# Kernel optimization log

Measured on AMD Instinct MI355X. Metric: run time of the kernel, lower is better.

Reference implementation:

```python
import jax, jax.numpy as jnp
import numpy as np
import math

EMBED = 512
HEADS = 2
HEAD_DIM = EMBED // HEADS
EPS = 1e-5

def layer_norm(x, g, b):
    mu = jnp.mean(x, axis=-1, keepdims=True)
    var = jnp.var(x, axis=-1, keepdims=True)
    return (x - mu) * jax.lax.rsqrt(var + EPS) * g + b

def setup_inputs() -> dict:
    key = jax.random.key(0)
    ks = jax.random.split(key, 16)
    s = 0.02
    inp = {
        "text_embeds": jax.random.normal(ks[0], (128, 32, EMBED), jnp.float32),
        "video_embeds": jax.random.normal(ks[1], (64, 12, EMBED), jnp.float32),
        "ln1_g": jnp.ones((EMBED,), jnp.float32),
        "ln1_b": jnp.zeros((EMBED,), jnp.float32),
        "Wq": jax.random.normal(ks[2], (EMBED, EMBED), jnp.float32) * s,
        "bq": jnp.zeros((EMBED,), jnp.float32),
        "Wk": jax.random.normal(ks[3], (EMBED, EMBED), jnp.float32) * s,
        "bk": jnp.zeros((EMBED,), jnp.float32),
        "Wv": jax.random.normal(ks[4], (EMBED, EMBED), jnp.float32) * s,
        "bv": jnp.zeros((EMBED,), jnp.float32),
        "Wo": jax.random.normal(ks[5], (EMBED, EMBED), jnp.float32) * s,
        "bo": jnp.zeros((EMBED,), jnp.float32),
        "Wl": jax.random.normal(ks[6], (EMBED, EMBED), jnp.float32) * s,
        "bl": jnp.zeros((EMBED,), jnp.float32),
        "ln2_g": jnp.ones((EMBED,), jnp.float32),
        "ln2_b": jnp.zeros((EMBED,), jnp.float32),
        "ln3_g": jnp.ones((EMBED,), jnp.float32),
        "ln3_b": jnp.zeros((EMBED,), jnp.float32),
    }
    return inp

def reference(text_embeds, video_embeds, ln1_g, ln1_b, Wq, bq, Wk, bk, Wv, bv,
              Wo, bo, Wl, bl, ln2_g, ln2_b, ln3_g, ln3_b):
    # shared layer_norm1 on both modalities
    t = layer_norm(text_embeds, ln1_g, ln1_b)    # [T, Nw, E]
    vd = layer_norm(video_embeds, ln1_g, ln1_b)  # [V, F, E]
    T, Nw, _ = t.shape
    V, Fr, _ = vd.shape
    q = (t @ Wq.T + bq).reshape(T, Nw, HEADS, HEAD_DIM)   # bthd
    k = (vd @ Wk.T + bk).reshape(V, Fr, HEADS, HEAD_DIM)  # avhd
    v = (vd @ Wv.T + bv).reshape(V, Fr, HEADS, HEAD_DIM)  # avhd
    # cross-modal outer-product attention logits: [V, T, H, F, Nw]
    logits = jnp.einsum('avhd,bthd->abhvt', k, q) / math.sqrt(HEAD_DIM)
    weights = jax.nn.softmax(logits, axis=3)  # softmax over frames
    attn = jnp.einsum('avhd,abhvt->abhtd', v, weights)  # [V, T, H, Nw, D]
    attn = attn.transpose(0, 1, 3, 2, 4).reshape(V, T, Nw, EMBED)
    attn = attn.mean(axis=0)                    # [T, Nw, E]
    o = attn @ Wo.T + bo
    o = layer_norm(o, ln2_g, ln2_b)
    lin = o @ Wl.T + bl  # dropout is identity in eval mode
    out = layer_norm(o + lin, ln3_g, ln3_b)
    return out
```

## Files before the change

kernel.cpp:

```cpp
#include <hip/hip_runtime.h>
#include <math.h>

#define EMBED 512
#define HD 256
#define FR 12
#define NV 64
#define NT_TOK 4096
#define NV_TOK 768

typedef __attribute__((ext_vector_type(8))) short short8;
typedef __attribute__((ext_vector_type(4))) float f32x4;

__device__ __forceinline__ unsigned int f2bf(float f) {
  unsigned int u = __float_as_uint(f);
  u += 0x7FFFu + ((u >> 16) & 1u);
  return u >> 16;
}
__device__ __forceinline__ void async_cp16(void* lds, const void* g) {
  __builtin_amdgcn_global_load_lds(
      (const __attribute__((address_space(1))) void*)g,
      (__attribute__((address_space(3))) void*)lds, 16, 0, 0);
}

__device__ __forceinline__ void gemm64_core(
    const unsigned short* __restrict__ Ab, int lda,
    const unsigned short* __restrict__ Bb, int ldb,
    int m0, int n0, int K,
    unsigned short* __restrict__ As, unsigned short* __restrict__ Bs,
    f32x4 acc[2][2]) {
  int tid = threadIdx.x;
  int w = tid >> 6, lane = tid & 63;
  int lr = lane & 15, quad = lane >> 4;
  int wm = (w >> 1) * 32, wn = (w & 1) * 32;
  int rowS[2], cgS[2];
  #pragma unroll
  for (int i = 0; i < 2; ++i) {
    int s = tid + i * 256;
    rowS[i] = s >> 3; cgS[i] = (s & 7) ^ (rowS[i] & 7);
  }
  int nk = K >> 6;
  #pragma unroll
  for (int i = 0; i < 2; ++i) {
    async_cp16(&As[(tid + i * 256) * 8],
               Ab + (size_t)(m0 + rowS[i]) * lda + cgS[i] * 8);
    async_cp16(&Bs[(tid + i * 256) * 8],
               Bb + (size_t)(n0 + rowS[i]) * ldb + cgS[i] * 8);
  }
  for (int k = 0; k < nk; ++k) {
    int cur = k & 1;
    __syncthreads();
    if (k + 1 < nk) {
      int nxt = cur ^ 1, koff = (k + 1) << 6;
      #pragma unroll
      for (int i = 0; i < 2; ++i) {
        async_cp16(&As[nxt * 4096 + (tid + i * 256) * 8],
                   Ab + (size_t)(m0 + rowS[i]) * lda + koff + cgS[i] * 8);
        async_cp16(&Bs[nxt * 4096 + (tid + i * 256) * 8],
                   Bb + (size_t)(n0 + rowS[i]) * ldb + koff + cgS[i] * 8);
      }
    }
    const unsigned short* Ac = As + cur * 4096;
    const unsigned short* Bc = Bs + cur * 4096;
    #pragma unroll
    for (int kk = 0; kk < 2; ++kk) {
      int sw = ((kk * 4 + quad) ^ (lr & 7)) * 8;
      short8 a0 = *(const short8*)&Ac[(wm + lr) * 64 + sw];
      short8 a1 = *(const short8*)&Ac[(wm + 16 + lr) * 64 + sw];
      short8 b0 = *(const short8*)&Bc[(wn + lr) * 64 + sw];
      short8 b1 = *(const short8*)&Bc[(wn + 16 + lr) * 64 + sw];
      acc[0][0] = __builtin_amdgcn_mfma_f32_16x16x32_bf16(a0, b0, acc[0][0], 0, 0, 0);
      acc[0][1] = __builtin_amdgcn_mfma_f32_16x16x32_bf16(a0, b1, acc[0][1], 0, 0, 0);
      acc[1][0] = __builtin_amdgcn_mfma_f32_16x16x32_bf16(a1, b0, acc[1][0], 0, 0, 0);
      acc[1][1] = __builtin_amdgcn_mfma_f32_16x16x32_bf16(a1, b1, acc[1][1], 0, 0, 0);
    }
  }
}

template <int MODE, bool BIAS>
__global__ __launch_bounds__(256, 4) void gemm64(
    const unsigned short* __restrict__ A, int lda, long AzS,
    const unsigned short* __restrict__ B, int ldb, long BzS,
    const float* __restrict__ bias, void* __restrict__ Cv, int ldc, long CzS,
    int K) {
  __shared__ __align__(16) unsigned short As[2 * 4096];
  __shared__ __align__(16) unsigned short Bs[2 * 4096];
  f32x4 acc[2][2] = {};
  const unsigned short* Ab = A + (size_t)blockIdx.z * AzS;
  const unsigned short* Bb = B + (size_t)blockIdx.z * BzS;
  int m0 = blockIdx.x * 64, n0 = blockIdx.y * 64;
  gemm64_core(Ab, lda, Bb, ldb, m0, n0, K, As, Bs, acc);
  int w = threadIdx.x >> 6, lane = threadIdx.x & 63;
  int lr = lane & 15, quad = lane >> 4;
  int wm = (w >> 1) * 32, wn = (w & 1) * 32;
  long cz = (long)blockIdx.z * CzS;
  #pragma unroll
  for (int j = 0; j < 2; ++j) {
    int col = n0 + wn + j * 16 + lr;
    float bv = BIAS ? bias[col] : 0.0f;
    #pragma unroll
    for (int i = 0; i < 2; ++i) {
      int rbase = m0 + wm + i * 16 + quad * 4;
      #pragma unroll
      for (int r = 0; r < 4; ++r) {
        float v = acc[i][j][r] + bv;
        if (MODE == 0)
          ((unsigned short*)Cv)[cz + (size_t)(rbase + r) * ldc + col] =
              (unsigned short)f2bf(v);
        else
          ((float*)Cv)[cz + (size_t)(rbase + r) * ldc + col] = v;
      }
    }
  }
}

__global__ __launch_bounds__(256, 4) void qkv_kernel(
    const unsigned short* __restrict__ tn, const unsigned short* __restrict__ vn,
    const unsigned short* __restrict__ Wq, const unsigned short* __restrict__ Wk,
    const unsigned short* __restrict__ Wv,
    const float* __restrict__ bq, const float* __restrict__ bk,
    const float* __restrict__ bv,
    unsigned short* __restrict__ Q, unsigned short* __restrict__ Kout,
    unsigned short* __restrict__ V) {
  __shared__ __align__(16) unsigned short As[2 * 4096];
  __shared__ __align__(16) unsigned short Bs[2 * 4096];
  int bid = blockIdx.x;
  const unsigned short *Ap, *Bp;
  const float* bias;
  unsigned short* outp;
  int m0, n0;
  if (bid < 512) {
    Ap = tn; Bp = Wq; bias = bq; outp = Q;
    m0 = (bid >> 3) * 64; n0 = (bid & 7) * 64;
  } else if (bid < 608) {
    int i = bid - 512;
    Ap = vn; Bp = Wk; bias = bk; outp = Kout;
    m0 = (i >> 3) * 64; n0 = (i & 7) * 64;
  } else {
    int i = bid - 608;
    Ap = vn; Bp = Wv; bias = bv; outp = V;
    m0 = (i >> 3) * 64; n0 = (i & 7) * 64;
  }
  f32x4 acc[2][2] = {};
  gemm64_core(Ap, EMBED, Bp, EMBED, m0, n0, EMBED, As, Bs, acc);
  int w = threadIdx.x >> 6, lane = threadIdx.x & 63;
  int lr = lane & 15, quad = lane >> 4;
  int wm = (w >> 1) * 32, wn = (w & 1) * 32;
  #pragma unroll
  for (int j = 0; j < 2; ++j) {
    int col = n0 + wn + j * 16 + lr;
    float bvv = bias[col];
    #pragma unroll
    for (int i = 0; i < 2; ++i) {
      int rbase = m0 + wm + i * 16 + quad * 4;
      #pragma unroll
      for (int r = 0; r < 4; ++r)
        outp[(size_t)(rbase + r) * EMBED + col] =
            (unsigned short)f2bf(acc[i][j][r] + bvv);
    }
  }
}

__global__ __launch_bounds__(256, 4) void sgemm_softmax(
    const unsigned short* __restrict__ Q, const unsigned short* __restrict__ Kb,
    const unsigned short* __restrict__ V, const unsigned short* __restrict__ Wo,
    unsigned short* __restrict__ P, unsigned short* __restrict__ W2) {
  __shared__ __align__(16) char smem[40960];
  int tid = threadIdx.x;
  int w = tid >> 6, lane = tid & 63;
  int lr = lane & 15, quad = lane >> 4;
  int bid = blockIdx.x;

  if (bid >= 1024) {
    int j = bid - 1024;
    int h = j / 96, i = j % 96;
    int m0 = (i / 12) * 64, n0 = (i % 12) * 64;
    unsigned short* As = (unsigned short*)smem;
    unsigned short* Bs = (unsigned short*)(smem + 16384);
    f32x4 acc[2][2] = {};
    gemm64_core(Wo + h * HD, EMBED, V + h * HD, EMBED, m0, n0, HD, As, Bs, acc);
    int wm = (w >> 1) * 32, wn = (w & 1) * 32;
    #pragma unroll
    for (int j2 = 0; j2 < 2; ++j2) {
      int col = n0 + wn + j2 * 16 + lr;
      #pragma unroll
      for (int i2 = 0; i2 < 2; ++i2) {
        int rbase = m0 + wm + i2 * 16 + quad * 4;
        #pragma unroll
        for (int r = 0; r < 4; ++r)
          W2[(size_t)(rbase + r) * 1536 + h * 768 + col] =
              (unsigned short)f2bf(acc[i2][j2][r]);
      }
    }
    return;
  }

  unsigned short* As = (unsigned short*)smem;
  unsigned short* Bs = (unsigned short*)(smem + 16384);
  int wm = (w >> 1) * 32, wn = (w & 1) * 48;
  int h = bid >> 9, rem = bid & 511;
  int m0 = (rem >> 3) * 64, n0 = (rem & 7) * 96;
  const unsigned short* Ab = Q + h * HD;
  const unsigned short* Bb = Kb + h * HD;
  int rowA[2], cgA[2], rowB[3], cgB[3];
  #pragma unroll
  for (int i = 0; i < 2; ++i) {
    int s = tid + i * 256;
    rowA[i] = s >> 3; cgA[i] = (s & 7) ^ (rowA[i] & 7);
  }
  #pragma unroll
  for (int i = 0; i < 3; ++i) {
    int s = tid + i * 256;
    rowB[i] = s >> 3; cgB[i] = (s & 7) ^ (rowB[i] & 7);
  }
  f32x4 acc[2][3] = {};
  const int nk = HD >> 6;
  #pragma unroll
  for (int i = 0; i < 2; ++i)
    async_cp16(&As[(tid + i * 256) * 8],
               Ab + (size_t)(m0 + rowA[i]) * EMBED + cgA[i] * 8);
  #pragma unroll
  for (int i = 0; i < 3; ++i)
    async_cp16(&Bs[(tid + i * 256) * 8],
               Bb + (size_t)(n0 + rowB[i]) * EMBED + cgB[i] * 8);
  for (int k = 0; k < nk; ++k) {
    int cur = k & 1;
    __syncthreads();
    if (k + 1 < nk) {
      int nxt = cur ^ 1, koff = (k + 1) << 6;
      #pragma unroll
      for (int i = 0; i < 2; ++i)
        async_cp16(&As[nxt * 4096 + (tid + i * 256) * 8],
                   Ab + (size_t)(m0 + rowA[i]) * EMBED + koff + cgA[i] * 8);
      #pragma unroll
      for (int i = 0; i < 3; ++i)
        async_cp16(&Bs[nxt * 6144 + (tid + i * 256) * 8],
                   Bb + (size_t)(n0 + rowB[i]) * EMBED + koff + cgB[i] * 8);
    }
    const unsigned short* Ac = As + cur * 4096;
    const unsigned short* Bc = Bs + cur * 6144;
    #pragma unroll
    for (int kk = 0; kk < 2; ++kk) {
      int sw = ((kk * 4 + quad) ^ (lr & 7)) * 8;
      short8 a0 = *(const short8*)&Ac[(wm + lr) * 64 + sw];
      short8 a1 = *(const short8*)&Ac[(wm + 16 + lr) * 64 + sw];
      short8 b0 = *(const short8*)&Bc[(wn + lr) * 64 + sw];
      short8 b1 = *(const short8*)&Bc[(wn + 16 + lr) * 64 + sw];
      short8 b2 = *(const short8*)&Bc[(wn + 32 + lr) * 64 + sw];
      acc[0][0] = __builtin_amdgcn_mfma_f32_16x16x32_bf16(a0, b0, acc[0][0], 0, 0, 0);
      acc[0][1] = __builtin_amdgcn_mfma_f32_16x16x32_bf16(a0, b1, acc[0][1], 0, 0, 0);
      acc[0][2] = __builtin_amdgcn_mfma_f32_16x16x32_bf16(a0, b2, acc[0][2], 0, 0, 0);
      acc[1][0] = __builtin_amdgcn_mfma_f32_16x16x32_bf16(a1, b0, acc[1][0], 0, 0, 0);
      acc[1][1] = __builtin_amdgcn_mfma_f32_16x16x32_bf16(a1, b1, acc[1][1], 0, 0, 0);
      acc[1][2] = __builtin_amdgcn_mfma_f32_16x16x32_bf16(a1, b2, acc[1][2], 0, 0, 0);
    }
  }
  __syncthreads();
  float* Sx = (float*)smem;
  #pragma unroll
  for (int j = 0; j < 3; ++j) {
    int col = wn + j * 16 + lr;
    #pragma unroll
    for (int i = 0; i < 2; ++i) {
      int rbase = wm + i * 16 + quad * 4;
      #pragma unroll
      for (int r = 0; r < 4; ++r) Sx[(rbase + r) * 100 + col] = acc[i][j][r];
    }
  }
  __syncthreads();
  #pragma unroll
  for (int gi = 0; gi < 2; ++gi) {
    int g = tid * 2 + gi;
    int row = g >> 3, gr = g & 7;
    const float* sp = Sx + row * 100 + gr * 12;
    float v[12];
    float m = -1e30f;
    #pragma unroll
    for (int f = 0; f < FR; ++f) { v[f] = sp[f] * 0.0625f; m = fmaxf(m, v[f]); }
    float s = 0.f;
    #pragma unroll
    for (int f = 0; f < FR; ++f) { v[f] = __expf(v[f] - m); s += v[f]; }
    float inv = (1.0f / NV) / s;
    unsigned short* pp =
        P + (size_t)(m0 + row) * 1536 + h * 768 + n0 + gr * 12;
    #pragma unroll
    for (int ii = 0; ii < 6; ++ii) {
      unsigned int lo = f2bf(v[2 * ii] * inv), hi = f2bf(v[2 * ii + 1] * inv);
      *(unsigned int*)(pp + 2 * ii) = lo | (hi << 16);
    }
  }
}

__device__ __forceinline__ void ln_row(
    const float* __restrict__ xr, const float* __restrict__ rr,
    const float* __restrict__ g, const float* __restrict__ b,
    float* __restrict__ outf, unsigned short* __restrict__ outb) {
  int t = threadIdx.x;
  float v0 = xr[t], v1 = xr[t + 256];
  if (rr != nullptr) { v0 += rr[t]; v1 += rr[t + 256]; }
  float s = v0 + v1;
  float s2 = v0 * v0 + v1 * v1;
  #pragma unroll
  for (int off = 32; off > 0; off >>= 1) {
    s += __shfl_down(s, off, 64);
    s2 += __shfl_down(s2, off, 64);
  }
  __shared__ float ss[4], ss2[4];
  __shared__ float mean_s, rstd_s;
  int wid = t >> 6;
  if ((t & 63) == 0) { ss[wid] = s; ss2[wid] = s2; }
  __syncthreads();
  if (t == 0) {
    float a = ss[0] + ss[1] + ss[2] + ss[3];
    float a2 = ss2[0] + ss2[1] + ss2[2] + ss2[3];
    float mean = a * (1.0f / EMBED);
    float var = a2 * (1.0f / EMBED) - mean * mean;
    mean_s = mean;
    rstd_s = rsqrtf(var + 1e-5f);
  }
  __syncthreads();
  float mean = mean_s, rstd = rstd_s;
  float y0 = (v0 - mean) * rstd * g[t] + b[t];
  float y1 = (v1 - mean) * rstd * g[t + 256] + b[t + 256];
  if (outf != nullptr) { outf[t] = y0; outf[t + 256] = y1; }
  if (outb != nullptr) {
    outb[t] = (unsigned short)f2bf(y0);
    outb[t + 256] = (unsigned short)f2bf(y1);
  }
}

__global__ __launch_bounds__(256) void ln_kernel(
    const float* __restrict__ x, const float* __restrict__ res,
    const float* __restrict__ g, const float* __restrict__ b,
    float* __restrict__ outf, unsigned short* __restrict__ outb) {
  size_t row = blockIdx.x;
  ln_row(x + row * EMBED, res ? res + row * EMBED : nullptr, g, b,
         outf ? outf + row * EMBED : nullptr,
         outb ? outb + row * EMBED : nullptr);
}

__global__ __launch_bounds__(256) void prep_kernel(
    const float* __restrict__ text, const float* __restrict__ video,
    const float* __restrict__ g, const float* __restrict__ b,
    const float* __restrict__ Wq, const float* __restrict__ Wk,
    const float* __restrict__ Wv, const float* __restrict__ Wo,
    const float* __restrict__ Wl, unsigned short* __restrict__ Wbf,
    unsigned short* __restrict__ tn, unsigned short* __restrict__ vn) {
  int bid = blockIdx.x;
  if (bid < 1280) {
    int i = bid * 256 + threadIdx.x;
    const float* srcs[5] = {Wq, Wk, Wv, Wo, Wl};
    const float* src = srcs[i >> 16];
    float4 v = ((const float4*)src)[i & 65535];
    uint2 o;
    o.x = f2bf(v.x) | (f2bf(v.y) << 16);
    o.y = f2bf(v.z) | (f2bf(v.w) << 16);
    ((uint2*)Wbf)[i] = o;
    return;
  }
  if (bid < 1280 + NT_TOK) {
    size_t row = bid - 1280;
    ln_row(text + row * EMBED, nullptr, g, b, nullptr, tn + row * EMBED);
  } else {
    size_t row = bid - (1280 + NT_TOK);
    ln_row(video + row * EMBED, nullptr, g, b, nullptr, vn + row * EMBED);
  }
}

extern "C" void kernel_launch(void* const* d_in, const int* in_sizes, int n_in,
                              void* d_out, int out_size, void* d_ws, size_t ws_size,
                              hipStream_t stream) {
  (void)in_sizes; (void)n_in; (void)out_size; (void)ws_size;
  const float* text  = (const float*)d_in[0];
  const float* video = (const float*)d_in[1];
  const float* ln1_g = (const float*)d_in[2];
  const float* ln1_b = (const float*)d_in[3];
  const float* Wq = (const float*)d_in[4];
  const float* bq = (const float*)d_in[5];
  const float* Wk = (const float*)d_in[6];
  const float* bk = (const float*)d_in[7];
  const float* Wv = (const float*)d_in[8];
  const float* bv = (const float*)d_in[9];
  const float* Wo = (const float*)d_in[10];
  const float* bo = (const float*)d_in[11];
  const float* Wl = (const float*)d_in[12];
  const float* bl = (const float*)d_in[13];
  const float* ln2_g = (const float*)d_in[14];
  const float* ln2_b = (const float*)d_in[15];
  const float* ln3_g = (const float*)d_in[16];
  const float* ln3_b = (const float*)d_in[17];
  float* out = (float*)d_out;

  char* base = (char*)d_ws;
  unsigned short* Wbf   = (unsigned short*)base;
  unsigned short* Wq_bf = Wbf + 0 * 262144;
  unsigned short* Wk_bf = Wbf + 1 * 262144;
  unsigned short* Wv_bf = Wbf + 2 * 262144;
  unsigned short* Wo_bf = Wbf + 3 * 262144;
  unsigned short* Wl_bf = Wbf + 4 * 262144;
  unsigned short* W2    = (unsigned short*)(base + 2621440);
  unsigned short* tn_bf = (unsigned short*)(base + 4194304);
  unsigned short* vn_bf = (unsigned short*)(base + 8388608);
  unsigned short* Q_bf  = (unsigned short*)(base + 9175040);
  unsigned short* K_bf  = (unsigned short*)(base + 13369344);
  unsigned short* V_bf  = (unsigned short*)(base + 14155776);
  unsigned short* P     = (unsigned short*)(base + 14942208);
  float* Ob  = (float*)(base + 4194304);
  float* o2f = (float*)(base + 14942208);
  unsigned short* o2_bf = (unsigned short*)(base + 23330816);
  float* lin = (float*)(base + 4194304);

  prep_kernel<<<1280 + NT_TOK + NV_TOK, 256, 0, stream>>>(
      text, video, ln1_g, ln1_b, Wq, Wk, Wv, Wo, Wl, Wbf, tn_bf, vn_bf);

  qkv_kernel<<<704, 256, 0, stream>>>(tn_bf, vn_bf, Wq_bf, Wk_bf, Wv_bf,
                                      bq, bk, bv, Q_bf, K_bf, V_bf);

  sgemm_softmax<<<1216, 256, 0, stream>>>(Q_bf, K_bf, V_bf, Wo_bf, P, W2);

  gemm64<1, true><<<dim3(64, 8, 1), 256, 0, stream>>>(
      P, 1536, 0, W2, 1536, 0, bo, Ob, EMBED, 0, 1536);

  ln_kernel<<<NT_TOK, 256, 0, stream>>>(Ob, nullptr, ln2_g, ln2_b, o2f, o2_bf);
  gemm64<1, true><<<dim3(64, 8, 1), 256, 0, stream>>>(
      o2_bf, EMBED, 0, Wl_bf, EMBED, 0, bl, lin, EMBED, 0, EMBED);
  ln_kernel<<<NT_TOK, 256, 0, stream>>>(o2f, lin, ln3_g, ln3_b, out, nullptr);
}
```

Before: 164.2 us.

## Fuse LN2 stats into Wo GEMM epilogue and LN2 apply into Wl GEMM

The Wo projection GEMM now accumulates per-row sum and sum-of-squares into a stats buffer with atomics, and the buffer is zeroed inside the QKV kernel. The Wl GEMM normalizes its fp32 input on the fly while staging the A tile, so the standalone LN2 kernel and its fp32/bf16 intermediates go away. The final LN3 kernel recomputes the LN2 output from Ob and the stats. This removes one launch and a full pass over activations, at the cost of global atomics, redundant LN2 work across the 8 column blocks, synchronous A-tile loads in the Wl GEMM, and a one-pass variance formula.

After: 161.5 us. About the same (-1.7%).

```diff
diff --git a/kernel.cpp b/kernel.cpp
--- a/kernel.cpp
+++ b/kernel.cpp
@@ -76,43 +76,6 @@
   }
 }
 
-template <int MODE, bool BIAS>
-__global__ __launch_bounds__(256, 4) void gemm64(
-    const unsigned short* __restrict__ A, int lda, long AzS,
-    const unsigned short* __restrict__ B, int ldb, long BzS,
-    const float* __restrict__ bias, void* __restrict__ Cv, int ldc, long CzS,
-    int K) {
-  __shared__ __align__(16) unsigned short As[2 * 4096];
-  __shared__ __align__(16) unsigned short Bs[2 * 4096];
-  f32x4 acc[2][2] = {};
-  const unsigned short* Ab = A + (size_t)blockIdx.z * AzS;
-  const unsigned short* Bb = B + (size_t)blockIdx.z * BzS;
-  int m0 = blockIdx.x * 64, n0 = blockIdx.y * 64;
-  gemm64_core(Ab, lda, Bb, ldb, m0, n0, K, As, Bs, acc);
-  int w = threadIdx.x >> 6, lane = threadIdx.x & 63;
-  int lr = lane & 15, quad = lane >> 4;
-  int wm = (w >> 1) * 32, wn = (w & 1) * 32;
-  long cz = (long)blockIdx.z * CzS;
-  #pragma unroll
-  for (int j = 0; j < 2; ++j) {
-    int col = n0 + wn + j * 16 + lr;
-    float bv = BIAS ? bias[col] : 0.0f;
-    #pragma unroll
-    for (int i = 0; i < 2; ++i) {
-      int rbase = m0 + wm + i * 16 + quad * 4;
-      #pragma unroll
-      for (int r = 0; r < 4; ++r) {
-        float v = acc[i][j][r] + bv;
-        if (MODE == 0)
-          ((unsigned short*)Cv)[cz + (size_t)(rbase + r) * ldc + col] =
-              (unsigned short)f2bf(v);
-        else
-          ((float*)Cv)[cz + (size_t)(rbase + r) * ldc + col] = v;
-      }
-    }
-  }
-}
-
 __global__ __launch_bounds__(256, 4) void qkv_kernel(
     const unsigned short* __restrict__ tn, const unsigned short* __restrict__ vn,
     const unsigned short* __restrict__ Wq, const unsigned short* __restrict__ Wk,
@@ -120,10 +83,11 @@
     const float* __restrict__ bq, const float* __restrict__ bk,
     const float* __restrict__ bv,
     unsigned short* __restrict__ Q, unsigned short* __restrict__ Kout,
-    unsigned short* __restrict__ V) {
+    unsigned short* __restrict__ V, float* __restrict__ stats) {
   __shared__ __align__(16) unsigned short As[2 * 4096];
   __shared__ __align__(16) unsigned short Bs[2 * 4096];
   int bid = blockIdx.x;
+  if (bid < 32) stats[bid * 256 + threadIdx.x] = 0.0f;
   const unsigned short *Ap, *Bp;
   const float* bias;
   unsigned short* outp;
@@ -280,8 +244,7 @@
     #pragma unroll
     for (int f = 0; f < FR; ++f) { v[f] = __expf(v[f] - m); s += v[f]; }
     float inv = (1.0f / NV) / s;
-    unsigned short* pp =
-        P + (size_t)(m0 + row) * 1536 + h * 768 + n0 + gr * 12;
+    unsigned short* pp = P + (size_t)(m0 + row) * 1536 + h * 768 + n0 + gr * 12;
     #pragma unroll
     for (int ii = 0; ii < 6; ++ii) {
       unsigned int lo = f2bf(v[2 * ii] * inv), hi = f2bf(v[2 * ii + 1] * inv);
@@ -290,13 +253,209 @@
   }
 }
 
+__global__ __launch_bounds__(256, 4) void gemm_pvo(
+    const unsigned short* __restrict__ P, const unsigned short* __restrict__ W2,
+    const float* __restrict__ bo, float* __restrict__ Ob,
+    float* __restrict__ stats) {
+  __shared__ __align__(16) unsigned short As[2 * 4096];
+  __shared__ __align__(16) unsigned short Bs[2 * 4096];
+  f32x4 acc[2][2] = {};
+  int m0 = blockIdx.x * 64, n0 = blockIdx.y * 64;
+  gemm64_core(P, 1536, W2, 1536, m0, n0, 1536, As, Bs, acc);
+  int w = threadIdx.x >> 6, lane = threadIdx.x & 63;
+  int lr = lane & 15, quad = lane >> 4;
+  int wm = (w >> 1) * 32, wn = (w & 1) * 32;
+  float rs[2][4] = {}, rq[2][4] = {};
+  #pragma unroll
+  for (int j = 0; j < 2; ++j) {
+    int col = n0 + wn + j * 16 + lr;
+    float bv = bo[col];
+    #pragma unroll
+    for (int i = 0; i < 2; ++i) {
+      int rbase = m0 + wm + i * 16 + quad * 4;
+      #pragma unroll
+      for (int r = 0; r < 4; ++r) {
+        float v = acc[i][j][r] + bv;
+        Ob[(size_t)(rbase + r) * EMBED + col] = v;
+        rs[i][r] += v;
+        rq[i][r] += v * v;
+      }
+    }
+  }
+  #pragma unroll
+  for (int off = 8; off > 0; off >>= 1) {
+    #pragma unroll
+    for (int i = 0; i < 2; ++i)
+      #pragma unroll
+      for (int r = 0; r < 4; ++r) {
+        rs[i][r] += __shfl_down(rs[i][r], off, 16);
+        rq[i][r] += __shfl_down(rq[i][r], off, 16);
+      }
+  }
+  if (lr == 0) {
+    #pragma unroll
+    for (int i = 0; i < 2; ++i) {
+      #pragma unroll
+      for (int r = 0; r < 4; ++r) {
+        int row = m0 + wm + i * 16 + quad * 4 + r;
+        atomicAdd(&stats[row * 2], rs[i][r]);
+        atomicAdd(&stats[row * 2 + 1], rq[i][r]);
+      }
+    }
+  }
+}
+
+__global__ __launch_bounds__(256) void gemm_lnl(
+    const float* __restrict__ Ob, const float* __restrict__ stats,
+    const float* __restrict__ g2, const float* __restrict__ b2,
+    const unsigned short* __restrict__ Wl, const float* __restrict__ bl,
+    float* __restrict__ lin) {
+  __shared__ __align__(16) unsigned short As[2 * 4096];
+  __shared__ __align__(16) unsigned short Bs[2 * 4096];
+  int tid = threadIdx.x;
+  int w = tid >> 6, lane = tid & 63;
+  int lr = lane & 15, quad = lane >> 4;
+  int wm = (w >> 1) * 32, wn = (w & 1) * 32;
+  int m0 = blockIdx.x * 64, n0 = blockIdx.y * 64;
+  int rowS[2], cgS[2];
+  float mu[2], rstd[2];
+  #pragma unroll
+  for (int i = 0; i < 2; ++i) {
+    int s = tid + i * 256;
+    rowS[i] = s >> 3; cgS[i] = (s & 7) ^ (rowS[i] & 7);
+    float s1 = stats[(m0 + rowS[i]) * 2];
+    float s2 = stats[(m0 + rowS[i]) * 2 + 1];
+    float m = s1 * (1.0f / EMBED);
+    mu[i] = m;
+    rstd[i] = rsqrtf(s2 * (1.0f / EMBED) - m * m + 1e-5f);
+  }
+  f32x4 acc[2][2] = {};
+  const int nk = EMBED >> 6;
+
+  #define STAGE_A(buf, koff)                                                  \
+    {                                                                         \
+      _Pragma("unroll") for (int i = 0; i < 2; ++i) {                         \
+        const float* src = Ob + (size_t)(m0 + rowS[i]) * EMBED + (koff) +     \
+                           cgS[i] * 8;                                        \
+        const float* gp = g2 + (koff) + cgS[i] * 8;                           \
+        const float* bp = b2 + (koff) + cgS[i] * 8;                           \
+        float4 x0 = *(const float4*)src;                                      \
+        float4 x1 = *(const float4*)(src + 4);                                \
+        float4 ga = *(const float4*)gp;                                       \
+        float4 gb = *(const float4*)(gp + 4);                                 \
+        float4 ba = *(const float4*)bp;                                       \
+        float4 bb = *(const float4*)(bp + 4);                                 \
+        float y0 = (x0.x - mu[i]) * rstd[i] * ga.x + ba.x;                    \
+        float y1 = (x0.y - mu[i]) * rstd[i] * ga.y + ba.y;                    \
+        float y2 = (x0.z - mu[i]) * rstd[i] * ga.z + ba.z;                    \
+        float y3 = (x0.w - mu[i]) * rstd[i] * ga.w + ba.w;                    \
+        float y4 = (x1.x - mu[i]) * rstd[i] * gb.x + bb.x;                    \
+        float y5 = (x1.y - mu[i]) * rstd[i] * gb.y + bb.y;                    \
+        float y6 = (x1.z - mu[i]) * rstd[i] * gb.z + bb.z;                    \
+        float y7 = (x1.w - mu[i]) * rstd[i] * gb.w + bb.w;                    \
+        uint4 pk;                                                             \
+        pk.x = f2bf(y0) | (f2bf(y1) << 16);                                   \
+        pk.y = f2bf(y2) | (f2bf(y3) << 16);                                   \
+        pk.z = f2bf(y4) | (f2bf(y5) << 16);                                   \
+        pk.w = f2bf(y6) | (f2bf(y7) << 16);                                   \
+        *(uint4*)&As[(buf)*4096 + (tid + i * 256) * 8] = pk;                  \
+      }                                                                       \
+    }
+
+  STAGE_A(0, 0)
+  #pragma unroll
+  for (int i = 0; i < 2; ++i)
+    async_cp16(&Bs[(tid + i * 256) * 8],
+               Wl + (size_t)(n0 + rowS[i]) * EMBED + cgS[i] * 8);
+  for (int k = 0; k < nk; ++k) {
+    int cur = k & 1;
+    __syncthreads();
+    if (k + 1 < nk) {
+      int nxt = cur ^ 1, koff = (k + 1) << 6;
+      STAGE_A(nxt, koff)
+      #pragma unroll
+      for (int i = 0; i < 2; ++i)
+        async_cp16(&Bs[nxt * 4096 + (tid + i * 256) * 8],
+                   Wl + (size_t)(n0 + rowS[i]) * EMBED + koff + cgS[i] * 8);
+    }
+    const unsigned short* Ac = As + cur * 4096;
+    const unsigned short* Bc = Bs + cur * 4096;
+    #pragma unroll
+    for (int kk = 0; kk < 2; ++kk) {
+      int sw = ((kk * 4 + quad) ^ (lr & 7)) * 8;
+      short8 a0 = *(const short8*)&Ac[(wm + lr) * 64 + sw];
+      short8 a1 = *(const short8*)&Ac[(wm + 16 + lr) * 64 + sw];
+      short8 b0 = *(const short8*)&Bc[(wn + lr) * 64 + sw];
+      short8 b1 = *(const short8*)&Bc[(wn + 16 + lr) * 64 + sw];
+      acc[0][0] = __builtin_amdgcn_mfma_f32_16x16x32_bf16(a0, b0, acc[0][0], 0, 0, 0);
+      acc[0][1] = __builtin_amdgcn_mfma_f32_16x16x32_bf16(a0, b1, acc[0][1], 0, 0, 0);
+      acc[1][0] = __builtin_amdgcn_mfma_f32_16x16x32_bf16(a1, b0, acc[1][0], 0, 0, 0);
+      acc[1][1] = __builtin_amdgcn_mfma_f32_16x16x32_bf16(a1, b1, acc[1][1], 0, 0, 0);
+    }
+  }
+  #pragma unroll
+  for (int j = 0; j < 2; ++j) {
+    int col = n0 + wn + j * 16 + lr;
+    float bv = bl[col];
+    #pragma unroll
+    for (int i = 0; i < 2; ++i) {
+      int rbase = m0 + wm + i * 16 + quad * 4;
+      #pragma unroll
+      for (int r = 0; r < 4; ++r)
+        lin[(size_t)(rbase + r) * EMBED + col] = acc[i][j][r] + bv;
+    }
+  }
+  #undef STAGE_A
+}
+
+__global__ __launch_bounds__(256) void ln3_kernel(
+    const float* __restrict__ Ob, const float* __restrict__ stats,
+    const float* __restrict__ lin,
+    const float* __restrict__ g2, const float* __restrict__ b2,
+    const float* __restrict__ g3, const float* __restrict__ b3,
+    float* __restrict__ out) {
+  int row = blockIdx.x;
+  int t = threadIdx.x;
+  float s1 = stats[row * 2], s2v = stats[row * 2 + 1];
+  float mu2 = s1 * (1.0f / EMBED);
+  float rstd2 = rsqrtf(s2v * (1.0f / EMBED) - mu2 * mu2 + 1e-5f);
+  const float* xr = Ob + (size_t)row * EMBED;
+  const float* lr_ = lin + (size_t)row * EMBED;
+  float v0 = (xr[t] - mu2) * rstd2 * g2[t] + b2[t] + lr_[t];
+  float v1 = (xr[t + 256] - mu2) * rstd2 * g2[t + 256] + b2[t + 256] + lr_[t + 256];
+  float s = v0 + v1;
+  float sq = v0 * v0 + v1 * v1;
+  #pragma unroll
+  for (int off = 32; off > 0; off >>= 1) {
+    s += __shfl_down(s, off, 64);
+    sq += __shfl_down(sq, off, 64);
+  }
+  __shared__ float ss[4], ss2[4];
+  __shared__ float mean_s, rstd_s;
+  int wid = t >> 6;
+  if ((t & 63) == 0) { ss[wid] = s; ss2[wid] = sq; }
+  __syncthreads();
+  if (t == 0) {
+    float a = ss[0] + ss[1] + ss[2] + ss[3];
+    float a2 = ss2[0] + ss2[1] + ss2[2] + ss2[3];
+    float mean = a * (1.0f / EMBED);
+    float var = a2 * (1.0f / EMBED) - mean * mean;
+    mean_s = mean;
+    rstd_s = rsqrtf(var + 1e-5f);
+  }
+  __syncthreads();
+  float mean = mean_s, rstd = rstd_s;
+  float* orow = out + (size_t)row * EMBED;
+  orow[t] = (v0 - mean) * rstd * g3[t] + b3[t];
+  orow[t + 256] = (v1 - mean) * rstd * g3[t + 256] + b3[t + 256];
+}
+
 __device__ __forceinline__ void ln_row(
-    const float* __restrict__ xr, const float* __restrict__ rr,
+    const float* __restrict__ xr,
     const float* __restrict__ g, const float* __restrict__ b,
-    float* __restrict__ outf, unsigned short* __restrict__ outb) {
+    unsigned short* __restrict__ outb) {
   int t = threadIdx.x;
   float v0 = xr[t], v1 = xr[t + 256];
-  if (rr != nullptr) { v0 += rr[t]; v1 += rr[t + 256]; }
   float s = v0 + v1;
   float s2 = v0 * v0 + v1 * v1;
   #pragma unroll
@@ -319,23 +478,9 @@
   }
   __syncthreads();
   float mean = mean_s, rstd = rstd_s;
-  float y0 = (v0 - mean) * rstd * g[t] + b[t];
-  float y1 = (v1 - mean) * rstd * g[t + 256] + b[t + 256];
-  if (outf != nullptr) { outf[t] = y0; outf[t + 256] = y1; }
-  if (outb != nullptr) {
-    outb[t] = (unsigned short)f2bf(y0);
-    outb[t + 256] = (unsigned short)f2bf(y1);
-  }
-}
-
-__global__ __launch_bounds__(256) void ln_kernel(
-    const float* __restrict__ x, const float* __restrict__ res,
-    const float* __restrict__ g, const float* __restrict__ b,
-    float* __restrict__ outf, unsigned short* __restrict__ outb) {
-  size_t row = blockIdx.x;
-  ln_row(x + row * EMBED, res ? res + row * EMBED : nullptr, g, b,
-         outf ? outf + row * EMBED : nullptr,
-         outb ? outb + row * EMBED : nullptr);
+  outb[t] = (unsigned short)f2bf((v0 - mean) * rstd * g[t] + b[t]);
+  outb[t + 256] =
+      (unsigned short)f2bf((v1 - mean) * rstd * g[t + 256] + b[t + 256]);
 }
 
 __global__ __launch_bounds__(256) void prep_kernel(
@@ -359,10 +504,10 @@
   }
   if (bid < 1280 + NT_TOK) {
     size_t row = bid - 1280;
-    ln_row(text + row * EMBED, nullptr, g, b, nullptr, tn + row * EMBED);
+    ln_row(text + row * EMBED, g, b, tn + row * EMBED);
   } else {
     size_t row = bid - (1280 + NT_TOK);
-    ln_row(video + row * EMBED, nullptr, g, b, nullptr, vn + row * EMBED);
+    ln_row(video + row * EMBED, g, b, vn + row * EMBED);
   }
 }
 
@@ -398,30 +543,29 @@
   unsigned short* Wo_bf = Wbf + 3 * 262144;
   unsigned short* Wl_bf = Wbf + 4 * 262144;
   unsigned short* W2    = (unsigned short*)(base + 2621440);
-  unsigned short* tn_bf = (unsigned short*)(base + 4194304);
-  unsigned short* vn_bf = (unsigned short*)(base + 8388608);
-  unsigned short* Q_bf  = (unsigned short*)(base + 9175040);
-  unsigned short* K_bf  = (unsigned short*)(base + 13369344);
-  unsigned short* V_bf  = (unsigned short*)(base + 14155776);
-  unsigned short* P     = (unsigned short*)(base + 14942208);
-  float* Ob  = (float*)(base + 4194304);
-  float* o2f = (float*)(base + 14942208);
-  unsigned short* o2_bf = (unsigned short*)(base + 23330816);
-  float* lin = (float*)(base + 4194304);
+  float*          stats = (float*)(base + 4194304);
+  unsigned short* tn_bf = (unsigned short*)(base + 4227072);
+  unsigned short* vn_bf = (unsigned short*)(base + 8421376);
+  unsigned short* Q_bf  = (unsigned short*)(base + 9207808);
+  unsigned short* K_bf  = (unsigned short*)(base + 13402112);
+  unsigned short* V_bf  = (unsigned short*)(base + 14188544);
+  unsigned short* P     = (unsigned short*)(base + 14974976);
+  float*          Ob    = (float*)(base + 27557888);
+  float*          lin   = (float*)(base + 35946496);
 
   prep_kernel<<<1280 + NT_TOK + NV_TOK, 256, 0, stream>>>(
       text, video, ln1_g, ln1_b, Wq, Wk, Wv, Wo, Wl, Wbf, tn_bf, vn_bf);
 
   qkv_kernel<<<704, 256, 0, stream>>>(tn_bf, vn_bf, Wq_bf, Wk_bf, Wv_bf,
-                                      bq, bk, bv, Q_bf, K_bf, V_bf);
+                                      bq, bk, bv, Q_bf, K_bf, V_bf, stats);
 
   sgemm_softmax<<<1216, 256, 0, stream>>>(Q_bf, K_bf, V_bf, Wo_bf, P, W2);
 
-  gemm64<1, true><<<dim3(64, 8, 1), 256, 0, stream>>>(
-      P, 1536, 0, W2, 1536, 0, bo, Ob, EMBED, 0, 1536);
-
-  ln_kernel<<<NT_TOK, 256, 0, stream>>>(Ob, nullptr, ln2_g, ln2_b, o2f, o2_bf);
-  gemm64<1, true><<<dim3(64, 8, 1), 256, 0, stream>>>(
-      o2_bf, EMBED, 0, Wl_bf, EMBED, 0, bl, lin, EMBED, 0, EMBED);
-  ln_kernel<<<NT_TOK, 256, 0, stream>>>(o2f, lin, ln3_g, ln3_b, out, nullptr);
-}
+  gemm_pvo<<<dim3(64, 8), 256, 0, stream>>>(P, W2, bo, Ob, stats);
+
+  gemm_lnl<<<dim3(64, 8), 256, 0, stream>>>(Ob, stats, ln2_g, ln2_b, Wl_bf,
+                                            bl, lin);
+
+  ln3_kernel<<<NT_TOK, 256, 0, stream>>>(Ob, stats, lin, ln2_g, ln2_b,
+                                         ln3_g, ln3_b, out);
+}
```
